# Kernel optimization log

Measured on AMD Instinct MI355X. Metric: run time of the kernel, lower is better.

## Reference

```python
import jax, jax.numpy as jnp
import numpy as np

B, S, D = 2, 2048, 768
H = 12
DH = D // H
EPS = 1e-12


def setup_inputs() -> dict:
    key = jax.random.key(0)
    ks = jax.random.split(key, 16)
    s = 0.02
    return {
        "hidden_states": jax.random.normal(ks[0], (B, S, D), jnp.float32),
        "attention_mask": jnp.zeros((B, 1, 1, S), jnp.float32),
        "position_bias": jax.random.normal(ks[1], (1, H, S, S), jnp.float32),
        "q_w": jax.random.normal(ks[2], (D, D), jnp.float32) * s,
        "q_b": jnp.zeros((D,), jnp.float32),
        "k_w": jax.random.normal(ks[3], (D, D), jnp.float32) * s,
        "k_b": jnp.zeros((D,), jnp.float32),
        "v_w": jax.random.normal(ks[4], (D, D), jnp.float32) * s,
        "v_b": jnp.zeros((D,), jnp.float32),
        "o_w": jax.random.normal(ks[5], (D, D), jnp.float32) * s,
        "o_b": jnp.zeros((D,), jnp.float32),
        "ln_w": jnp.ones((D,), jnp.float32),
        "ln_b": jnp.zeros((D,), jnp.float32),
    }


def _split_heads(x):
    # [B, S, D] -> [B, H, S, DH]
    b, s, _ = x.shape
    return x.reshape(b, s, H, DH).transpose(0, 2, 1, 3)


def reference(hidden_states, attention_mask, position_bias,
              q_w, q_b, k_w, k_b, v_w, v_b, o_w, o_b, ln_w, ln_b):
    # nn.Linear: y = x @ W.T + b (W stored [out, in])
    q = _split_heads(hidden_states @ q_w.T + q_b)
    k = _split_heads(hidden_states @ k_w.T + k_b)
    v = _split_heads(hidden_states @ v_w.T + v_b)

    scale = 1.0 / jnp.sqrt(jnp.asarray(DH, hidden_states.dtype))
    scores = jnp.einsum('bhqd,bhkd->bhqk', q, k) * scale
    scores = scores + position_bias + attention_mask
    probs = jax.nn.softmax(scores, axis=-1)

    c = jnp.einsum('bhqk,bhkd->bhqd', probs, v)
    c = c.transpose(0, 2, 1, 3).reshape(hidden_states.shape[0], -1, D)
    o = c @ o_w.T + o_b

    # residual + LayerNorm (dropout is identity at eval)
    x = o + hidden_states
    mu = jnp.mean(x, axis=-1, keepdims=True)
    var = jnp.mean(jnp.square(x - mu), axis=-1, keepdims=True)
    out = (x - mu) * jax.lax.rsqrt(var + EPS) * ln_w + ln_b
    return out
```

## Files before the change

kernel.cpp:

```cpp
#include <hip/hip_runtime.h>
#include <math.h>

typedef unsigned short u16;
typedef float f32x4 __attribute__((ext_vector_type(4)));
typedef __bf16 bf16x8 __attribute__((ext_vector_type(8)));

#define B_ 2
#define S_ 2048
#define D_ 768
#define H_ 12
#define DH_ 64

__device__ __forceinline__ u16 f2bf(float x) {
  union { float f; unsigned u; } v; v.f = x;
  unsigned r = v.u + 0x7fffu + ((v.u >> 16) & 1u);
  return (u16)(r >> 16);
}

__device__ __forceinline__ f32x4 zero4() { f32x4 z = {0.f, 0.f, 0.f, 0.f}; return z; }

__device__ __forceinline__ f32x4 mfma16(bf16x8 a, bf16x8 b, f32x4 c) {
  return __builtin_amdgcn_mfma_f32_16x16x32_bf16(a, b, c, 0, 0, 0);
}

__device__ __forceinline__ void gload_lds16(const void* g, void* l) {
  __builtin_amdgcn_global_load_lds((const __attribute__((address_space(1))) void*)g,
                                   (__attribute__((address_space(3))) void*)l, 16, 0, 0);
}

__global__ void cvt_kernel(const float* __restrict__ hid, const float* __restrict__ qw,
                           const float* __restrict__ kw, const float* __restrict__ vw,
                           const float* __restrict__ ow, u16* __restrict__ Hb,
                           u16* __restrict__ Wb) {
  const int NH = B_ * S_ * D_;
  const int NW = D_ * D_;
  const int T4 = (NH + 4 * NW) >> 2;
  int stride = gridDim.x * blockDim.x;
  for (int i = blockIdx.x * blockDim.x + threadIdx.x; i < T4; i += stride) {
    int e = i << 2;
    const float* src; u16* dst;
    if (e < NH) { src = hid + e; dst = Hb + e; }
    else {
      int o = e - NH;
      int m = o / NW, oo = o - m * NW;
      src = (m == 0 ? qw : m == 1 ? kw : m == 2 ? vw : ow) + oo;
      dst = Wb + o;
    }
    f32x4 v = *(const f32x4*)src;
    uint2 o2;
    o2.x = (unsigned)f2bf(v[0]) | ((unsigned)f2bf(v[1]) << 16);
    o2.y = (unsigned)f2bf(v[2]) | ((unsigned)f2bf(v[3]) << 16);
    *(uint2*)dst = o2;
  }
}

#define BM 128
#define BN 128
#define BK 64

__global__ __launch_bounds__(256) void gemm_kernel(
    const u16* __restrict__ A, const u16* __restrict__ W,
    const float* __restrict__ bq, const float* __restrict__ bk, const float* __restrict__ bv,
    u16* __restrict__ Qb, u16* __restrict__ Kb, u16* __restrict__ Vtmp,
    float* __restrict__ Of, const float* __restrict__ bO, int mode)
{
  __shared__ __align__(16) u16 As[BM * BK];
  __shared__ __align__(16) u16 Bs[BN * BK];
  int t = threadIdx.x;
  int lane = t & 63, w = t >> 6;
  int wr = w >> 1, wc = w & 1;
  int l15 = lane & 15, l4 = lane >> 4;
  int m0 = blockIdx.y * BM, n0 = blockIdx.x * BN;

  f32x4 acc[4][4];
#pragma unroll
  for (int i = 0; i < 4; ++i)
#pragma unroll
    for (int j = 0; j < 4; ++j) acc[i][j] = zero4();

  const int K = D_;
  for (int k0 = 0; k0 < K; k0 += BK) {
    __syncthreads();
#pragma unroll
    for (int p = 0; p < 4; ++p) {
      int seg = p * 4 + w;
      int bd = seg * 64 + lane;
      int row = bd >> 3;
      int slot = (bd & 7) ^ (row & 7);
      gload_lds16(A + (size_t)(m0 + row) * K + k0 + slot * 8, (char*)As + seg * 1024);
      gload_lds16(W + (size_t)(n0 + row) * K + k0 + slot * 8, (char*)Bs + seg * 1024);
    }
    __syncthreads();
#pragma unroll
    for (int kk = 0; kk < 2; ++kk) {
      bf16x8 af[4], bfr[4];
#pragma unroll
      for (int i = 0; i < 4; ++i) {
        int ra = wr * 64 + i * 16 + l15;
        af[i] = *(const bf16x8*)((const char*)As + ra * 128 +
                                 ((kk * 64 + (l4 << 4)) ^ ((ra & 7) << 4)));
        int rb = wc * 64 + i * 16 + l15;
        bfr[i] = *(const bf16x8*)((const char*)Bs + rb * 128 +
                                  ((kk * 64 + (l4 << 4)) ^ ((rb & 7) << 4)));
      }
#pragma unroll
      for (int i = 0; i < 4; ++i)
#pragma unroll
        for (int j = 0; j < 4; ++j)
          acc[i][j] = mfma16(af[i], bfr[j], acc[i][j]);
    }
  }

  if (mode == 0) {
    int mat = n0 / D_;
    int ncol0 = (n0 - mat * D_) + wc * 64;
    const float* bias = (mat == 0) ? bq : (mat == 1 ? bk : bv);
    u16* outp = (mat == 0) ? Qb : (mat == 1 ? Kb : Vtmp);
    float scale = (mat == 0) ? 0.125f : 1.0f;
    int h = ncol0 >> 6;
#pragma unroll
    for (int j = 0; j < 4; ++j) {
      int d = j * 16 + l15;
      float bvv = bias[ncol0 + d];
#pragma unroll
      for (int i = 0; i < 4; ++i) {
#pragma unroll
        for (int r = 0; r < 4; ++r) {
          int m = m0 + wr * 64 + i * 16 + (l4 << 2) + r;
          int bb = m >> 11, ss = m & 2047;
          float val = (acc[i][j][r] + bvv) * scale;
          outp[(((size_t)bb * H_ + h) * S_ + ss) * DH_ + d] = f2bf(val);
        }
      }
    }
  } else {
#pragma unroll
    for (int j = 0; j < 4; ++j) {
      int n = n0 + wc * 64 + j * 16 + l15;
      float bvv = bO[n];
#pragma unroll
      for (int i = 0; i < 4; ++i) {
#pragma unroll
        for (int r = 0; r < 4; ++r) {
          int m = m0 + wr * 64 + i * 16 + (l4 << 2) + r;
          Of[(size_t)m * D_ + n] = acc[i][j][r] + bvv;
        }
      }
    }
  }
}

__global__ __launch_bounds__(256) void vtrans_kernel(const u16* __restrict__ V,
                                                     u16* __restrict__ Vt) {
  __shared__ __align__(16) u16 tile[64 * 64];
  int t = threadIdx.x;
  int s0 = blockIdx.x * 64;
  int bh = blockIdx.y;
  const u16* src = V + ((size_t)bh * S_ + s0) * DH_;
#pragma unroll
  for (int p = 0; p < 2; ++p) {
    int bd = t + p * 256;
    int row = bd >> 3, slot = bd & 7;
    uint4 v = *(const uint4*)(src + row * 64 + slot * 8);
    *(uint4*)((char*)tile + row * 128 + ((slot ^ (row & 7)) << 4)) = v;
  }
  __syncthreads();
  int d = t >> 2, sc = (t & 3) * 16;
  u16* dst = Vt + ((size_t)bh * DH_ + d) * S_ + s0 + sc;
  int colB = d * 2;
#pragma unroll
  for (int half = 0; half < 2; ++half) {
    u16 tmp[8] __attribute__((aligned(16)));
#pragma unroll
    for (int j = 0; j < 8; ++j) {
      int s = sc + half * 8 + j;
      tmp[j] = *(const u16*)((const char*)tile + s * 128 +
                             (((colB >> 4) ^ (s & 7)) << 4) + (colB & 15));
    }
    *(uint4*)(dst + half * 8) = *(const uint4*)tmp;
  }
}

__global__ __launch_bounds__(512, 4) void attn_kernel(
    const u16* __restrict__ Qb, const u16* __restrict__ Kb, const u16* __restrict__ Vt,
    const float* __restrict__ bias, const float* __restrict__ mask, u16* __restrict__ Cb)
{
  __shared__ __align__(16) u16 Ks[2][64 * 64];
  __shared__ __align__(16) u16 Vs[2][64 * 64];
  __shared__ __align__(16) char Bls[2][16384];
  __shared__ __align__(16) u16 Ps[4][16][72];
  float (*Osh)[16][66] = (float (*)[16][66])&Bls[0][0];
  float (*Lsh)[2][16] = (float (*)[2][16])(&Bls[0][0] + 16896);

  int t = threadIdx.x, lane = t & 63, w = t >> 6;
  int qg = w & 3, kg = w >> 2;
  int q0 = blockIdx.x * 64, h = blockIdx.y, b = blockIdx.z;
  size_t bh = (size_t)b * H_ + h;
  const u16* Qp = Qb + (bh * S_ + q0) * DH_;
  const u16* Kp = Kb + bh * S_ * DH_;
  const u16* Vp = Vt + bh * DH_ * S_;
  const float* biasp = bias + ((size_t)h * S_ + q0) * S_;
  const float* maskp = mask + (size_t)b * S_;
  int l15 = lane & 15, l4 = lane >> 4;
  int kc0 = kg * 32;

  bf16x8 qf0, qf1;
  {
    const u16* qrow = Qp + (qg * 16 + l15) * DH_;
    qf0 = *(const bf16x8*)(qrow + l4 * 8);
    qf1 = *(const bf16x8*)(qrow + 32 + l4 * 8);
  }

  f32x4 oacc[4];
#pragma unroll
  for (int i = 0; i < 4; ++i) oacc[i] = zero4();
  float lrow[4] = {0.f, 0.f, 0.f, 0.f};

  auto STAGE_KV = [&](int kt, int sb) {
    int row = t >> 3;
    int slot = (t & 7) ^ (row & 7);
    gload_lds16(Kp + (size_t)(kt * 64 + row) * DH_ + slot * 8, (char*)Ks[sb] + w * 1024);
    gload_lds16(Vp + (size_t)row * S_ + kt * 64 + slot * 8, (char*)Vs[sb] + w * 1024);
  };
  auto STAGE_BIAS = [&](int kt, int bb) {
    int k0 = kt * 64;
#pragma unroll
    for (int p = 0; p < 2; ++p) {
      int seg = p * 8 + w;
      int row = seg * 4 + (lane >> 4);
      int byt = ((lane & 15) << 4) ^ ((row & 7) << 4);
      gload_lds16((const char*)(biasp + (size_t)row * S_ + k0) + byt,
                  &Bls[bb][0] + seg * 1024);
    }
  };

  float mcur[2], mnxt[2];

  STAGE_KV(0, 0);
  STAGE_BIAS(0, 0);
#pragma unroll
  for (int kf = 0; kf < 2; ++kf) mcur[kf] = maskp[kc0 + kf * 16 + l15];
  __syncthreads();

  for (int kt = 0; kt < S_ / 64; ++kt) {
    if (kt + 1 < S_ / 64) {
      STAGE_KV(kt + 1, (kt + 1) & 1);
      STAGE_BIAS(kt + 1, (kt + 1) & 1);
#pragma unroll
      for (int kf = 0; kf < 2; ++kf)
        mnxt[kf] = maskp[(kt + 1) * 64 + kc0 + kf * 16 + l15];
    }

    const u16* Kc = Ks[kt & 1];
    const u16* Vc = Vs[kt & 1];
    const char* Bc = &Bls[kt & 1][0];

    float bcv[2][4];
#pragma unroll
    for (int kf = 0; kf < 2; ++kf) {
      int col = kc0 + kf * 16 + l15;
#pragma unroll
      for (int r = 0; r < 4; ++r) {
        int row = qg * 16 + (l4 << 2) + r;
        bcv[kf][r] = *(const float*)(Bc + row * 256 + ((col << 2) ^ ((row & 7) << 4)));
      }
    }

    f32x4 sf[2];
#pragma unroll
    for (int kf = 0; kf < 2; ++kf) {
      int row = kc0 + kf * 16 + l15;
      bf16x8 kb0 = *(const bf16x8*)((const char*)Kc + row * 128 +
                                    ((l4 << 4) ^ ((row & 7) << 4)));
      bf16x8 kb1 = *(const bf16x8*)((const char*)Kc + row * 128 +
                                    ((64 + (l4 << 4)) ^ ((row & 7) << 4)));
      f32x4 s0 = zero4();
      s0 = mfma16(qf0, kb0, s0);
      s0 = mfma16(qf1, kb1, s0);
      sf[kf] = s0;
    }

#pragma unroll
    for (int kf = 0; kf < 2; ++kf) {
      float p0 = __expf(sf[kf][0] + bcv[kf][0] + mcur[kf]);
      float p1 = __expf(sf[kf][1] + bcv[kf][1] + mcur[kf]);
      float p2 = __expf(sf[kf][2] + bcv[kf][2] + mcur[kf]);
      float p3 = __expf(sf[kf][3] + bcv[kf][3] + mcur[kf]);
      sf[kf][0] = p0; sf[kf][1] = p1; sf[kf][2] = p2; sf[kf][3] = p3;
      lrow[0] += p0; lrow[1] += p1; lrow[2] += p2; lrow[3] += p3;
    }

#pragma unroll
    for (int r = 0; r < 4; ++r)
#pragma unroll
      for (int kf = 0; kf < 2; ++kf)
        Ps[qg][(l4 << 2) + r][kc0 + kf * 16 + l15] = f2bf(sf[kf][r]);

    bf16x8 pa = *(const bf16x8*)&Ps[qg][l15][kc0 + l4 * 8];

#pragma unroll
    for (int df = 0; df < 4; ++df) {
      int row = df * 16 + l15;
      bf16x8 vb = *(const bf16x8*)((const char*)Vc + row * 128 +
                                   ((kg * 64 + (l4 << 4)) ^ ((row & 7) << 4)));
      oacc[df] = mfma16(pa, vb, oacc[df]);
    }

    __syncthreads();
    mcur[0] = mnxt[0]; mcur[1] = mnxt[1];
  }

#pragma unroll
  for (int r = 0; r < 4; ++r) {
#pragma unroll
    for (int o = 1; o < 16; o <<= 1) lrow[r] += __shfl_xor(lrow[r], o, 64);
  }
  if (l15 == 0) {
#pragma unroll
    for (int r = 0; r < 4; ++r) Lsh[qg][kg][(l4 << 2) + r] = lrow[r];
  }
  if (kg == 1) {
#pragma unroll
    for (int r = 0; r < 4; ++r)
#pragma unroll
      for (int df = 0; df < 4; ++df)
        Osh[qg][(l4 << 2) + r][df * 16 + l15] = oacc[df][r];
  }
  __syncthreads();
  if (kg == 0) {
#pragma unroll
    for (int r = 0; r < 4; ++r) {
      int rr = (l4 << 2) + r;
      float inv = 1.0f / (Lsh[qg][0][rr] + Lsh[qg][1][rr]);
      int q = q0 + qg * 16 + rr;
      size_t base = ((size_t)b * S_ + q) * D_ + h * DH_ + l15;
#pragma unroll
      for (int df = 0; df < 4; ++df)
        Cb[base + df * 16] = f2bf((oacc[df][r] + Osh[qg][rr][df * 16 + l15]) * inv);
    }
  }
}

__global__ __launch_bounds__(192) void ln_kernel(const float* __restrict__ O,
                                                 const float* __restrict__ hid,
                                                 const float* __restrict__ lw,
                                                 const float* __restrict__ lb,
                                                 float* __restrict__ out) {
  int row = blockIdx.x, t = threadIdx.x;
  size_t base = (size_t)row * D_;
  f32x4 x = *(const f32x4*)(O + base + t * 4);
  f32x4 hh = *(const f32x4*)(hid + base + t * 4);
  x = x + hh;
  float s = x[0] + x[1] + x[2] + x[3];
  float s2 = x[0] * x[0] + x[1] * x[1] + x[2] * x[2] + x[3] * x[3];
#pragma unroll
  for (int o = 1; o < 64; o <<= 1) {
    s += __shfl_xor(s, o, 64);
    s2 += __shfl_xor(s2, o, 64);
  }
  __shared__ float rs[3], rs2[3];
  int w = t >> 6, lane = t & 63;
  if (lane == 0) { rs[w] = s; rs2[w] = s2; }
  __syncthreads();
  s = rs[0] + rs[1] + rs[2];
  s2 = rs2[0] + rs2[1] + rs2[2];
  float mu = s * (1.0f / 768.0f);
  float var = s2 * (1.0f / 768.0f) - mu * mu;
  float rstd = rsqrtf(var + 1e-12f);
  f32x4 w4 = *(const f32x4*)(lw + t * 4);
  f32x4 b4 = *(const f32x4*)(lb + t * 4);
  f32x4 y = (x - mu) * rstd * w4 + b4;
  *(f32x4*)(out + base + t * 4) = y;
}

extern "C" void kernel_launch(void* const* d_in, const int* in_sizes, int n_in,
                              void* d_out, int out_size, void* d_ws, size_t ws_size,
                              hipStream_t stream) {
  const float* hid  = (const float*)d_in[0];
  const float* mask = (const float*)d_in[1];
  const float* bias = (const float*)d_in[2];
  const float* qw = (const float*)d_in[3];
  const float* qb = (const float*)d_in[4];
  const float* kw = (const float*)d_in[5];
  const float* kb = (const float*)d_in[6];
  const float* vw = (const float*)d_in[7];
  const float* vb = (const float*)d_in[8];
  const float* ow = (const float*)d_in[9];
  const float* ob = (const float*)d_in[10];
  const float* lnw = (const float*)d_in[11];
  const float* lnb = (const float*)d_in[12];

  char* ws = (char*)d_ws;
  const size_t NHB = (size_t)B_ * S_ * D_ * 2;
  const size_t NWB = (size_t)4 * D_ * D_ * 2;
  const size_t NQB = (size_t)B_ * H_ * S_ * DH_ * 2;
  u16* Hb = (u16*)ws;
  u16* Wb = (u16*)(ws + NHB);
  u16* Qb = (u16*)(ws + NHB + NWB);
  u16* Kb = (u16*)(ws + NHB + NWB + NQB);
  u16* Vt = (u16*)(ws + NHB + NWB + 2 * NQB);
  u16* Cb = (u16*)(ws + NHB + NWB + 3 * NQB);
  float* Of = (float*)(ws + NHB + NWB + 4 * NQB);
  u16* Vtmp = (u16*)Of;

  cvt_kernel<<<2048, 256, 0, stream>>>(hid, qw, kw, vw, ow, Hb, Wb);

  gemm_kernel<<<dim3(18, 32), 256, 0, stream>>>(
      Hb, Wb, qb, kb, vb, Qb, Kb, Vtmp, nullptr, nullptr, 0);

  vtrans_kernel<<<dim3(S_ / 64, B_ * H_), 256, 0, stream>>>(Vtmp, Vt);

  attn_kernel<<<dim3(S_ / 64, H_, B_), 512, 0, stream>>>(Qb, Kb, Vt, bias, mask, Cb);

  gemm_kernel<<<dim3(6, 32), 256, 0, stream>>>(
      Cb, Wb + (size_t)3 * D_ * D_, nullptr, nullptr, nullptr,
      nullptr, nullptr, nullptr, Of, ob, 1);

  ln_kernel<<<B_ * S_, 192, 0, stream>>>(Of, hid, lnw, lnb, (float*)d_out);
}
```

Before: 173.0 us.

## Prepack exp(position bias) as bf16 in MFMA fragment order for attention

Adds a prepack kernel that reads the fp32 position bias once, computes exp(bias), rounds it to bf16, and stores it in per-lane fragment order. The attention kernel then loads one 16-byte vector per lane per tile straight into registers and multiplies it into exp(score+mask). This replaces the LDS staging of fp32 bias, which both batches previously read separately, and frees LDS so occupancy can be raised (launch bounds 4 to 6). Costs are an extra pass over the bias, bf16 precision loss in the bias factor, overflow risk if exp(bias) is large, and workspace aliasing: Of now overlaps pbuf and Cb overlaps Hb.

```diff
diff --git a/kernel.cpp b/kernel.cpp
--- a/kernel.cpp
+++ b/kernel.cpp
@@ -54,6 +54,45 @@
   }
 }
 
+__global__ __launch_bounds__(256) void prepack_kernel(const float* __restrict__ bias,
+                                                      u16* __restrict__ pb) {
+  __shared__ __align__(16) u16 bl[4][2056];
+  int x = blockIdx.x;
+  int band = x & 15, qt = (x >> 4) & 31, h = x >> 9;
+  int t = threadIdx.x;
+  const float* src = bias + ((size_t)h * S_ + qt * 64 + band * 4) * S_;
+#pragma unroll
+  for (int p = 0; p < 8; ++p) {
+    int e = p * 1024 + t * 4;
+    f32x4 v = *(const f32x4*)(src + e);
+    u16 a0 = f2bf(__expf(v[0])), a1 = f2bf(__expf(v[1]));
+    u16 a2 = f2bf(__expf(v[2])), a3 = f2bf(__expf(v[3]));
+    int row = e >> 11, col = e & 2047;
+    uint2 pk;
+    pk.x = (unsigned)a0 | ((unsigned)a1 << 16);
+    pk.y = (unsigned)a2 | ((unsigned)a3 << 16);
+    *(uint2*)&bl[row][col] = pk;
+  }
+  __syncthreads();
+  int qg = band >> 2, l4 = band & 3;
+  int w_ = t >> 6, lane_ = t & 63;
+  size_t obase = ((size_t)h * 32 + qt) * 32 * 4096;
+#pragma unroll
+  for (int i = 0; i < 4; ++i) {
+    int id = w_ * 256 + i * 64 + lane_;
+    int kt = id >> 5, rem = id & 31;
+    int kg = rem >> 4, l15 = rem & 15;
+    u16 vals[8] __attribute__((aligned(16)));
+#pragma unroll
+    for (int kf = 0; kf < 2; ++kf)
+#pragma unroll
+      for (int r = 0; r < 4; ++r)
+        vals[kf * 4 + r] = bl[r][kt * 64 + kg * 32 + kf * 16 + l15];
+    int w = kg * 4 + qg, lane = l4 * 16 + l15;
+    *(uint4*)(pb + obase + (size_t)kt * 4096 + (w * 64 + lane) * 8) = *(const uint4*)vals;
+  }
+}
+
 #define BM 128
 #define BN 128
 #define BK 64
@@ -181,16 +220,16 @@
   }
 }
 
-__global__ __launch_bounds__(512, 4) void attn_kernel(
+__global__ __launch_bounds__(512, 6) void attn_kernel(
     const u16* __restrict__ Qb, const u16* __restrict__ Kb, const u16* __restrict__ Vt,
-    const float* __restrict__ bias, const float* __restrict__ mask, u16* __restrict__ Cb)
+    const u16* __restrict__ pb, const float* __restrict__ mask, u16* __restrict__ Cb)
 {
   __shared__ __align__(16) u16 Ks[2][64 * 64];
   __shared__ __align__(16) u16 Vs[2][64 * 64];
-  __shared__ __align__(16) char Bls[2][16384];
-  __shared__ __align__(16) u16 Ps[4][16][72];
-  float (*Osh)[16][66] = (float (*)[16][66])&Bls[0][0];
-  float (*Lsh)[2][16] = (float (*)[2][16])(&Bls[0][0] + 16896);
+  __shared__ __align__(16) char upool[17408];
+  u16 (*Ps)[16][72] = (u16 (*)[16][72])upool;
+  float (*Osh)[16][66] = (float (*)[16][66])upool;
+  float (*Lsh)[2][16] = (float (*)[2][16])(upool + 16896);
 
   int t = threadIdx.x, lane = t & 63, w = t >> 6;
   int qg = w & 3, kg = w >> 2;
@@ -199,10 +238,11 @@
   const u16* Qp = Qb + (bh * S_ + q0) * DH_;
   const u16* Kp = Kb + bh * S_ * DH_;
   const u16* Vp = Vt + bh * DH_ * S_;
-  const float* biasp = bias + ((size_t)h * S_ + q0) * S_;
   const float* maskp = mask + (size_t)b * S_;
   int l15 = lane & 15, l4 = lane >> 4;
   int kc0 = kg * 32;
+
+  const u16* pbp = pb + ((size_t)h * 32 + blockIdx.x) * 32 * 4096 + (w * 64 + lane) * 8;
 
   bf16x8 qf0, qf1;
   {
@@ -222,22 +262,12 @@
     gload_lds16(Kp + (size_t)(kt * 64 + row) * DH_ + slot * 8, (char*)Ks[sb] + w * 1024);
     gload_lds16(Vp + (size_t)row * S_ + kt * 64 + slot * 8, (char*)Vs[sb] + w * 1024);
   };
-  auto STAGE_BIAS = [&](int kt, int bb) {
-    int k0 = kt * 64;
-#pragma unroll
-    for (int p = 0; p < 2; ++p) {
-      int seg = p * 8 + w;
-      int row = seg * 4 + (lane >> 4);
-      int byt = ((lane & 15) << 4) ^ ((row & 7) << 4);
-      gload_lds16((const char*)(biasp + (size_t)row * S_ + k0) + byt,
-                  &Bls[bb][0] + seg * 1024);
-    }
-  };
-
+
+  uint4 pbc, pbn;
   float mcur[2], mnxt[2];
 
   STAGE_KV(0, 0);
-  STAGE_BIAS(0, 0);
+  pbc = *(const uint4*)pbp;
 #pragma unroll
   for (int kf = 0; kf < 2; ++kf) mcur[kf] = maskp[kc0 + kf * 16 + l15];
   __syncthreads();
@@ -245,7 +275,7 @@
   for (int kt = 0; kt < S_ / 64; ++kt) {
     if (kt + 1 < S_ / 64) {
       STAGE_KV(kt + 1, (kt + 1) & 1);
-      STAGE_BIAS(kt + 1, (kt + 1) & 1);
+      pbn = *(const uint4*)(pbp + (size_t)(kt + 1) * 4096);
 #pragma unroll
       for (int kf = 0; kf < 2; ++kf)
         mnxt[kf] = maskp[(kt + 1) * 64 + kc0 + kf * 16 + l15];
@@ -253,18 +283,6 @@
 
     const u16* Kc = Ks[kt & 1];
     const u16* Vc = Vs[kt & 1];
-    const char* Bc = &Bls[kt & 1][0];
-
-    float bcv[2][4];
-#pragma unroll
-    for (int kf = 0; kf < 2; ++kf) {
-      int col = kc0 + kf * 16 + l15;
-#pragma unroll
-      for (int r = 0; r < 4; ++r) {
-        int row = qg * 16 + (l4 << 2) + r;
-        bcv[kf][r] = *(const float*)(Bc + row * 256 + ((col << 2) ^ ((row & 7) << 4)));
-      }
-    }
 
     f32x4 sf[2];
 #pragma unroll
@@ -280,14 +298,18 @@
       sf[kf] = s0;
     }
 
-#pragma unroll
-    for (int kf = 0; kf < 2; ++kf) {
-      float p0 = __expf(sf[kf][0] + bcv[kf][0] + mcur[kf]);
-      float p1 = __expf(sf[kf][1] + bcv[kf][1] + mcur[kf]);
-      float p2 = __expf(sf[kf][2] + bcv[kf][2] + mcur[kf]);
-      float p3 = __expf(sf[kf][3] + bcv[kf][3] + mcur[kf]);
-      sf[kf][0] = p0; sf[kf][1] = p1; sf[kf][2] = p2; sf[kf][3] = p3;
-      lrow[0] += p0; lrow[1] += p1; lrow[2] += p2; lrow[3] += p3;
+    {
+      const u16* ps = (const u16*)&pbc;
+#pragma unroll
+      for (int kf = 0; kf < 2; ++kf) {
+#pragma unroll
+        for (int r = 0; r < 4; ++r) {
+          float pbf = __uint_as_float((unsigned)ps[kf * 4 + r] << 16);
+          float p = __expf(sf[kf][r] + mcur[kf]) * pbf;
+          sf[kf][r] = p;
+          lrow[r] += p;
+        }
+      }
     }
 
 #pragma unroll
@@ -307,6 +329,7 @@
     }
 
     __syncthreads();
+    pbc = pbn;
     mcur[0] = mnxt[0]; mcur[1] = mnxt[1];
   }
 
@@ -391,26 +414,28 @@
   const float* lnb = (const float*)d_in[12];
 
   char* ws = (char*)d_ws;
-  const size_t NHB = (size_t)B_ * S_ * D_ * 2;
-  const size_t NWB = (size_t)4 * D_ * D_ * 2;
-  const size_t NQB = (size_t)B_ * H_ * S_ * DH_ * 2;
+  const size_t SZ6 = (size_t)B_ * S_ * D_ * 2;
+  const size_t SZW = (size_t)4 * D_ * D_ * 2;
   u16* Hb = (u16*)ws;
-  u16* Wb = (u16*)(ws + NHB);
-  u16* Qb = (u16*)(ws + NHB + NWB);
-  u16* Kb = (u16*)(ws + NHB + NWB + NQB);
-  u16* Vt = (u16*)(ws + NHB + NWB + 2 * NQB);
-  u16* Cb = (u16*)(ws + NHB + NWB + 3 * NQB);
-  float* Of = (float*)(ws + NHB + NWB + 4 * NQB);
-  u16* Vtmp = (u16*)Of;
+  u16* Cb = (u16*)ws;
+  u16* Wb = (u16*)(ws + SZ6);
+  u16* Qb = (u16*)(ws + SZ6 + SZW);
+  u16* Kb = (u16*)(ws + 2 * SZ6 + SZW);
+  u16* Vt = (u16*)(ws + 3 * SZ6 + SZW);
+  u16* Vtmp = (u16*)(ws + 4 * SZ6 + SZW);
+  u16* pbuf = (u16*)(ws + 5 * SZ6 + SZW);
+  float* Of = (float*)(ws + 5 * SZ6 + SZW);
 
   cvt_kernel<<<2048, 256, 0, stream>>>(hid, qw, kw, vw, ow, Hb, Wb);
+
+  prepack_kernel<<<6144, 256, 0, stream>>>(bias, pbuf);
 
   gemm_kernel<<<dim3(18, 32), 256, 0, stream>>>(
       Hb, Wb, qb, kb, vb, Qb, Kb, Vtmp, nullptr, nullptr, 0);
 
   vtrans_kernel<<<dim3(S_ / 64, B_ * H_), 256, 0, stream>>>(Vtmp, Vt);
 
-  attn_kernel<<<dim3(S_ / 64, H_, B_), 512, 0, stream>>>(Qb, Kb, Vt, bias, mask, Cb);
+  attn_kernel<<<dim3(S_ / 64, H_, B_), 512, 0, stream>>>(Qb, Kb, Vt, pbuf, mask, Cb);
 
   gemm_kernel<<<dim3(6, 32), 256, 0, stream>>>(
       Cb, Wb + (size_t)3 * D_ * D_, nullptr, nullptr, nullptr,
```

After: 186.6 us. 7.9% more time.
